# Optimization experiments

Measured on AMD Instinct MI355X. Metric: run time of the kernel, lower is better.

## Reference

```python
import jax, jax.numpy as jnp
import numpy as np

BATCH = 8
NDATA = 8192
NPOINT = 1024
NSAMPLE = 32
RADIUS = 0.2
CFEAT = 64


def setup_inputs() -> dict:
    key = jax.random.key(0)
    k1, k2, k3 = jax.random.split(key, 3)
    new_xyz = jax.random.normal(k1, (BATCH, NPOINT, 3), dtype=jnp.float32)
    xyz = jax.random.normal(k2, (BATCH, NDATA, 3), dtype=jnp.float32)
    points = jax.random.normal(k3, (BATCH, NDATA, CFEAT), dtype=jnp.float32)
    return {"new_xyz": new_xyz, "xyz": xyz, "points": points}


def reference(new_xyz, xyz, points):
    # Pairwise distances from every centroid to every dataset point.
    # delta: [B, P, N, 3]
    delta = xyz[:, None, :, :] - new_xyz[:, :, None, :]
    dist = jnp.linalg.norm(delta, axis=-1)  # [B, P, N]

    # Sort by distance (the original does a full argsort per centroid).
    sorted_idx = jnp.argsort(dist, axis=-1).astype(jnp.int32)  # [B, P, N]
    sorted_d = jnp.take_along_axis(dist, sorted_idx, axis=-1)  # [B, P, N]

    # Nearest point index replaces out-of-radius slots.
    nearest = sorted_idx[:, :, 0:1]  # [B, P, 1]
    radius_idx = jnp.where(sorted_d < RADIUS, sorted_idx, nearest)
    idx = radius_idx[:, :, :NSAMPLE]  # [B, P, S] int32 (ndataset >= nsample)

    # Batched gathers: grouped_xyz [B, P, S, 3], grouped_points [B, P, S, C].
    grouped_xyz = jnp.take_along_axis(
        xyz[:, None, :, :], idx[..., None], axis=2)
    grouped_points = jnp.take_along_axis(
        points[:, None, :, :], idx[..., None], axis=2)
    new_points = jnp.concatenate([grouped_xyz, grouped_points], axis=-1)
    return (new_points, idx, grouped_xyz)
```

## Files before the change

kernel.cpp:

```cpp
#include <hip/hip_runtime.h>
#include <math.h>

typedef unsigned int   u32;
typedef unsigned long long u64;

#define BATCH   8
#define NDATA   8192
#define NPOINT  1024
#define NSAMPLE 32
#define CFEAT   64
#define ROWF    67
#define MAXCAND 128
#define QPB     4
#define TILE    512
#define DWT     (TILE*3)
#define NT      (NDATA/TILE)
#define PLANE   516

#define OUT_IDX (BATCH*NPOINT*NSAMPLE*ROWF)
#define OUT_GX  (OUT_IDX + BATCH*NPOINT*NSAMPLE)

__device__ __forceinline__ float rnbf(float f) {
    u32 b = __float_as_uint(f);
    b += 0x7FFFu + ((b >> 16) & 1u);
    return __uint_as_float(b & 0xFFFF0000u);
}
__device__ __forceinline__ int clampidx(int v) {
    return (v < 0) ? 0 : (v > NDATA-1 ? NDATA-1 : v);
}

__global__ __launch_bounds__(256, 8)
void grouping_kernel(const float* __restrict__ new_xyz,
                     const float* __restrict__ xyz,
                     const float* __restrict__ points,
                     float* __restrict__ out, float T)
{
    __shared__ __align__(16) float S[2][3*PLANE];
    __shared__ float cand_s[QPB][MAXCAND];
    __shared__ int   cand_i[QPB][MAXCAND];
    __shared__ int   sel[QPB][NSAMPLE];

    const int tid  = threadIdx.x;
    const int wv   = tid >> 6;
    const int lane = tid & 63;
    const int q    = blockIdx.x * QPB + wv;
    const int b    = q >> 10;

    if (lane < NSAMPLE) sel[wv][lane] = 0;

    const float qx = new_xyz[q*3 + 0];
    const float qy = new_xyz[q*3 + 1];
    const float qz = new_xyz[q*3 + 2];
    const float* bx = xyz + (size_t)b * NDATA * 3;

    #pragma unroll
    for (int k = 0; k < DWT/256; ++k) {
        int w = k*256 + tid;
        int p = w / 3, c = w - 3*p;
        S[0][c*PLANE + p] = bx[w];
    }
    __syncthreads();

    int n = 0;
    for (int t = 0; t < NT; ++t) {
        const int cur = t & 1, nxt = cur ^ 1;
        if (t + 1 < NT) {
            #pragma unroll
            for (int k = 0; k < DWT/256; ++k) {
                int w = k*256 + tid;
                int p = w / 3, c = w - 3*p;
                S[nxt][c*PLANE + p] = bx[(t+1)*DWT + w];
            }
        }
        #pragma unroll
        for (int u = 0; u < TILE/256; ++u) {
            const float4 xv = ((const float4*)(S[cur]          ))[u*64 + lane];
            const float4 yv = ((const float4*)(S[cur] +   PLANE))[u*64 + lane];
            const float4 zv = ((const float4*)(S[cur] + 2*PLANE))[u*64 + lane];
            #pragma unroll
            for (int j = 0; j < 4; ++j) {
                float dx = __fsub_rn((&xv.x)[j], qx);
                float dy = __fsub_rn((&yv.x)[j], qy);
                float dz = __fsub_rn((&zv.x)[j], qz);
                float d2 = __fadd_rn(__fadd_rn(__fmul_rn(dx,dx), __fmul_rn(dy,dy)),
                                     __fmul_rn(dz,dz));
                bool cc = d2 < T;
                u64 m = __ballot(cc);
                if (m) {
                    if (cc) {
                        int below = __builtin_amdgcn_mbcnt_hi((u32)(m >> 32),
                                     __builtin_amdgcn_mbcnt_lo((u32)m, 0));
                        int pos = n + below;
                        if (pos < MAXCAND) {
                            cand_s[wv][pos] = __fsqrt_rn(d2);
                            cand_i[wv][pos] = t*TILE + u*256 + 4*lane + j;
                        }
                    }
                    n += (int)__popcll(m);
                }
            }
        }
        __syncthreads();
    }

    int mini = 0;
    if (n == 0) {
        float mind = 3.402823466e38f; int mi = 0;
        for (int k = 0; k < NDATA/64; ++k) {
            int i = (k << 6) + lane;
            float dx = __fsub_rn(bx[i*3+0], qx);
            float dy = __fsub_rn(bx[i*3+1], qy);
            float dz = __fsub_rn(bx[i*3+2], qz);
            float d2 = __fadd_rn(__fadd_rn(__fmul_rn(dx,dx), __fmul_rn(dy,dy)),
                                 __fmul_rn(dz,dz));
            if (d2 < mind) { mind = d2; mi = i; }
        }
        float ms = __fsqrt_rn(mind);
        for (int off = 32; off; off >>= 1) {
            float os = __shfl_xor(ms, off);
            int   oi = __shfl_xor(mi, off);
            if (os < ms || (os == ms && oi < mi)) { ms = os; mi = oi; }
        }
        mini = mi;
    }

    __syncthreads();

    const int nj = n > MAXCAND ? MAXCAND : n;
    for (int kk = lane; kk < nj; kk += 64) {
        float sk = cand_s[wv][kk];
        int   ik = cand_i[wv][kk];
        int r = 0;
        for (int mm = 0; mm < nj; ++mm) {
            float sm = cand_s[wv][mm];
            int   im = cand_i[wv][mm];
            r += (int)((sm < sk) | ((sm == sk) & (im < ik)));
        }
        if (r < NSAMPLE) sel[wv][r] = clampidx(ik);
    }
    __syncthreads();
    {
        const int nsel = nj < NSAMPLE ? nj : NSAMPLE;
        if (lane >= nsel && lane < NSAMPLE) {
            int pad = (nj > 0) ? sel[wv][0] : clampidx(mini);
            sel[wv][lane] = pad;
        }
    }
    __syncthreads();

    if (lane < NSAMPLE)
        out[OUT_IDX + (size_t)q*NSAMPLE + lane] = rnbf((float)sel[wv][lane]);

    for (int e = lane; e < NSAMPLE*3; e += 64) {
        int sR = e / 3, c2 = e - sR*3;
        int is = sel[wv][sR];
        out[OUT_GX + (size_t)q*(NSAMPLE*3) + e] = rnbf(bx[is*3 + c2]);
    }

    const float* prow = points + (size_t)b * NDATA * CFEAT;
    float* onp = out + (size_t)q * (NSAMPLE*ROWF);
    for (int e = lane; e < NSAMPLE*ROWF; e += 64) {
        int sR = e / ROWF;
        int c2 = e - sR*ROWF;
        int is = sel[wv][sR];
        const float* ap = (c2 < 3) ? (bx + (size_t)is*3 + c2)
                                   : (prow + (size_t)is*CFEAT + (c2-3));
        onp[e] = rnbf(*ap);
    }
}

extern "C" void kernel_launch(void* const* d_in, const int* in_sizes, int n_in,
                              void* d_out, int out_size, void* d_ws, size_t ws_size,
                              hipStream_t stream) {
    union { u32 u; float f; } lo, hi, mid;
    lo.u = 0u; hi.f = 0.05f;
    while (hi.u - lo.u > 1u) {
        mid.u = lo.u + (hi.u - lo.u) / 2u;
        if (sqrtf(mid.f) >= 0.2f) hi.u = mid.u; else lo.u = mid.u;
    }
    float T = hi.f;

    grouping_kernel<<<(BATCH*NPOINT)/QPB, 256, 0, stream>>>(
        (const float*)d_in[0],
        (const float*)d_in[1],
        (const float*)d_in[2],
        (float*)d_out, T);
}
```

Measured before the change: 131.6 us.

## Bin dataset points into x-slabs so each query scans only nearby points

Adds a pre-pass kernel that counting-sorts each batch's points into 256 buckets along x. It writes SoA coordinates, the original indices and bucket offsets to the workspace. The grouping kernel then scans only the buckets within radius of the query's x, instead of streaming all 8192 points through shared memory with block-wide syncs. This costs an extra launch and a small serial prefix scan, and candidate insertion order now depends on atomic ordering. Ties are still broken by index, so results stay deterministic unless a query has more than the maximum number of candidates.

```diff
diff --git a/kernel.cpp b/kernel.cpp
--- a/kernel.cpp
+++ b/kernel.cpp
@@ -12,10 +12,7 @@
 #define ROWF    67
 #define MAXCAND 128
 #define QPB     4
-#define TILE    512
-#define DWT     (TILE*3)
-#define NT      (NDATA/TILE)
-#define PLANE   516
+#define NB      256
 
 #define OUT_IDX (BATCH*NPOINT*NSAMPLE*ROWF)
 #define OUT_GX  (OUT_IDX + BATCH*NPOINT*NSAMPLE)
@@ -28,14 +25,49 @@
 __device__ __forceinline__ int clampidx(int v) {
     return (v < 0) ? 0 : (v > NDATA-1 ? NDATA-1 : v);
 }
+__device__ __forceinline__ int xbucket(float v) {
+    int c = (int)floorf((v + 4.5f) * 28.444445f);
+    return c < 0 ? 0 : (c > NB-1 ? NB-1 : c);
+}
+
+__global__ __launch_bounds__(256)
+void bin_kernel(const float* __restrict__ xyz,
+                float* __restrict__ wxs, float* __restrict__ wys,
+                float* __restrict__ wzs, u32* __restrict__ wid,
+                u32* __restrict__ wst)
+{
+    __shared__ u32 cnt[NB], cur[NB];
+    const int b = blockIdx.x, tid = threadIdx.x;
+    const float* bx = xyz + (size_t)b * NDATA * 3;
+    cnt[tid] = 0;
+    __syncthreads();
+    for (int p = tid; p < NDATA; p += 256)
+        atomicAdd(&cnt[xbucket(bx[p*3])], 1u);
+    __syncthreads();
+    if (tid == 0) {
+        u32 acc = 0;
+        for (int c = 0; c < NB; ++c) { u32 v = cnt[c]; cnt[c] = acc; cur[c] = acc; acc += v; }
+    }
+    __syncthreads();
+    wst[b*(NB+1) + tid] = cnt[tid];
+    if (tid == 0) wst[b*(NB+1) + NB] = NDATA;
+    for (int p = tid; p < NDATA; p += 256) {
+        float x = bx[p*3], y = bx[p*3+1], z = bx[p*3+2];
+        u32 pos = atomicAdd(&cur[xbucket(x)], 1u);
+        wxs[b*NDATA+pos] = x; wys[b*NDATA+pos] = y; wzs[b*NDATA+pos] = z;
+        wid[b*NDATA+pos] = (u32)p;
+    }
+}
 
 __global__ __launch_bounds__(256, 8)
 void grouping_kernel(const float* __restrict__ new_xyz,
                      const float* __restrict__ xyz,
                      const float* __restrict__ points,
+                     const float* __restrict__ wxs, const float* __restrict__ wys,
+                     const float* __restrict__ wzs, const u32* __restrict__ wid,
+                     const u32* __restrict__ wst,
                      float* __restrict__ out, float T)
 {
-    __shared__ __align__(16) float S[2][3*PLANE];
     __shared__ float cand_s[QPB][MAXCAND];
     __shared__ int   cand_i[QPB][MAXCAND];
     __shared__ int   sel[QPB][NSAMPLE];
@@ -51,56 +83,41 @@
     const float qx = new_xyz[q*3 + 0];
     const float qy = new_xyz[q*3 + 1];
     const float qz = new_xyz[q*3 + 2];
-    const float* bx = xyz + (size_t)b * NDATA * 3;
-
-    #pragma unroll
-    for (int k = 0; k < DWT/256; ++k) {
-        int w = k*256 + tid;
-        int p = w / 3, c = w - 3*p;
-        S[0][c*PLANE + p] = bx[w];
-    }
-    __syncthreads();
+    const float* bx  = xyz + (size_t)b * NDATA * 3;
+    const float* xs  = wxs + (size_t)b * NDATA;
+    const float* ys  = wys + (size_t)b * NDATA;
+    const float* zs  = wzs + (size_t)b * NDATA;
+    const u32*   ids = wid + (size_t)b * NDATA;
+
+    const int blo = xbucket(__fsub_rn(qx, 0.2005f));
+    const int bhi = xbucket(__fadd_rn(qx, 0.2005f));
+    const u32 j0 = wst[b*(NB+1) + blo];
+    const u32 j1 = wst[b*(NB+1) + bhi + 1];
 
     int n = 0;
-    for (int t = 0; t < NT; ++t) {
-        const int cur = t & 1, nxt = cur ^ 1;
-        if (t + 1 < NT) {
-            #pragma unroll
-            for (int k = 0; k < DWT/256; ++k) {
-                int w = k*256 + tid;
-                int p = w / 3, c = w - 3*p;
-                S[nxt][c*PLANE + p] = bx[(t+1)*DWT + w];
-            }
-        }
-        #pragma unroll
-        for (int u = 0; u < TILE/256; ++u) {
-            const float4 xv = ((const float4*)(S[cur]          ))[u*64 + lane];
-            const float4 yv = ((const float4*)(S[cur] +   PLANE))[u*64 + lane];
-            const float4 zv = ((const float4*)(S[cur] + 2*PLANE))[u*64 + lane];
-            #pragma unroll
-            for (int j = 0; j < 4; ++j) {
-                float dx = __fsub_rn((&xv.x)[j], qx);
-                float dy = __fsub_rn((&yv.x)[j], qy);
-                float dz = __fsub_rn((&zv.x)[j], qz);
-                float d2 = __fadd_rn(__fadd_rn(__fmul_rn(dx,dx), __fmul_rn(dy,dy)),
-                                     __fmul_rn(dz,dz));
-                bool cc = d2 < T;
-                u64 m = __ballot(cc);
-                if (m) {
-                    if (cc) {
-                        int below = __builtin_amdgcn_mbcnt_hi((u32)(m >> 32),
-                                     __builtin_amdgcn_mbcnt_lo((u32)m, 0));
-                        int pos = n + below;
-                        if (pos < MAXCAND) {
-                            cand_s[wv][pos] = __fsqrt_rn(d2);
-                            cand_i[wv][pos] = t*TILE + u*256 + 4*lane + j;
-                        }
-                    }
-                    n += (int)__popcll(m);
+    for (u32 jb = j0; jb < j1; jb += 64) {
+        u32 j  = jb + lane;
+        bool in = j < j1;
+        u32 jj = in ? j : (j1 - 1);
+        float dx = __fsub_rn(xs[jj], qx);
+        float dy = __fsub_rn(ys[jj], qy);
+        float dz = __fsub_rn(zs[jj], qz);
+        float d2 = __fadd_rn(__fadd_rn(__fmul_rn(dx,dx), __fmul_rn(dy,dy)),
+                             __fmul_rn(dz,dz));
+        bool cc = in && (d2 < T);
+        u64 m = __ballot(cc);
+        if (m) {
+            if (cc) {
+                int below = __builtin_amdgcn_mbcnt_hi((u32)(m >> 32),
+                             __builtin_amdgcn_mbcnt_lo((u32)m, 0));
+                int pos = n + below;
+                if (pos < MAXCAND) {
+                    cand_s[wv][pos] = __fsqrt_rn(d2);
+                    cand_i[wv][pos] = (int)ids[jj];
                 }
             }
-        }
-        __syncthreads();
+            n += (int)__popcll(m);
+        }
     }
 
     int mini = 0;
@@ -180,9 +197,17 @@
     }
     float T = hi.f;
 
+    float* wxs = (float*)d_ws;
+    float* wys = wxs + BATCH*NDATA;
+    float* wzs = wys + BATCH*NDATA;
+    u32*   wid = (u32*)(wzs + BATCH*NDATA);
+    u32*   wst = wid + BATCH*NDATA;
+
+    const float* nxz = (const float*)d_in[0];
+    const float* xyz = (const float*)d_in[1];
+    const float* pts = (const float*)d_in[2];
+
+    bin_kernel<<<BATCH, 256, 0, stream>>>(xyz, wxs, wys, wzs, wid, wst);
     grouping_kernel<<<(BATCH*NPOINT)/QPB, 256, 0, stream>>>(
-        (const float*)d_in[0],
-        (const float*)d_in[1],
-        (const float*)d_in[2],
-        (float*)d_out, T);
-}
+        nxz, xyz, pts, wxs, wys, wzs, wid, wst, (float*)d_out, T);
+}
```

After: 154.5 us. 17.4% more time.
